# Performance work log

Measured on AMD Instinct MI355X. Metric: run time of the kernel, lower is better.

Reference implementation:

```python
import jax, jax.numpy as jnp
import numpy as np

D_IN = 768
D_OUT = 768
NUM_HEADS = 12
HEAD_DIM = D_OUT // NUM_HEADS
SEQ = 4096
BATCH = 1


def setup_inputs() -> dict:
    key = jax.random.key(0)
    ks = jax.random.split(key, 6)
    s = 1.0 / np.sqrt(D_IN)
    return {
        "x": jax.random.normal(ks[0], (BATCH, SEQ, D_IN), dtype=jnp.float32),
        "W_query": jax.random.normal(ks[1], (D_IN, D_OUT), dtype=jnp.float32) * s,
        "W_key": jax.random.normal(ks[2], (D_IN, D_OUT), dtype=jnp.float32) * s,
        "W_value": jax.random.normal(ks[3], (D_IN, D_OUT), dtype=jnp.float32) * s,
        "W_out": jax.random.normal(ks[4], (D_OUT, D_OUT), dtype=jnp.float32) * s,
        "b_out": jax.random.normal(ks[5], (D_OUT,), dtype=jnp.float32) * 0.01,
    }


def reference(x, W_query, W_key, W_value, W_out, b_out):
    B, S, _ = x.shape
    # QKV projections (qkv_bias=False)
    q = (x @ W_query).reshape(B, S, NUM_HEADS, HEAD_DIM)
    k = (x @ W_key).reshape(B, S, NUM_HEADS, HEAD_DIM)
    v = (x @ W_value).reshape(B, S, NUM_HEADS, HEAD_DIM)
    # attention scores [B, H, S, S] with causal mask
    scores = jnp.einsum("bqhd,bkhd->bhqk", q, k) / jnp.sqrt(
        jnp.asarray(HEAD_DIM, dtype=x.dtype)
    )
    causal = jnp.tril(jnp.ones((S, S), dtype=bool))
    scores = jnp.where(causal, scores, jnp.finfo(x.dtype).min)
    attn = jax.nn.softmax(scores, axis=-1)  # dropout p=0.0 -> identity
    ctx = jnp.einsum("bhqk,bkhd->bqhd", attn, v).reshape(B, S, D_OUT)
    return ctx @ W_out + b_out
```

## Files before the change

kernel.cpp:

```cpp
#include <hip/hip_runtime.h>
#include <stdint.h>

#define SEQ 4096
#define DM 768
#define NH 12
#define HD 64

typedef __attribute__((ext_vector_type(8))) short bf8;
typedef __attribute__((ext_vector_type(4))) float f4;
typedef __attribute__((ext_vector_type(16))) float f32x16;

static __device__ __forceinline__ f4 mfma_bf16(bf8 a, bf8 b, f4 c) {
  return __builtin_amdgcn_mfma_f32_16x16x32_bf16(a, b, c, 0, 0, 0);
}
static __device__ __forceinline__ f32x16 mfma32(bf8 a, bf8 b, f32x16 c) {
  return __builtin_amdgcn_mfma_f32_32x32x16_bf16(a, b, c, 0, 0, 0);
}

static __device__ __forceinline__ unsigned short f2bf(float f) {
  unsigned int u = __float_as_uint(f);
  u += 0x7FFFu + ((u >> 16) & 1u);
  return (unsigned short)(u >> 16);
}

static __device__ __forceinline__ unsigned int cvtpk(float lo, float hi) {
  unsigned int r;
  asm("v_cvt_pk_bf16_f32 %0, %1, %2" : "=v"(r) : "v"(lo), "v"(hi));
  return r;
}

static __device__ __forceinline__ void gload_lds16(const void* g, void* l) {
  __builtin_amdgcn_global_load_lds(
      (const __attribute__((address_space(1))) void*)g,
      (__attribute__((address_space(3))) void*)l, 16, 0, 0);
}

__global__ __launch_bounds__(256) void k_cvt(const float* __restrict__ x,
                                             unsigned short* __restrict__ xb) {
  int i = (blockIdx.x * 256 + threadIdx.x) * 4;
  float4 v = *reinterpret_cast<const float4*>(x + i);
  ushort4 o;
  o.x = f2bf(v.x); o.y = f2bf(v.y); o.z = f2bf(v.z); o.w = f2bf(v.w);
  *reinterpret_cast<ushort4*>(xb + i) = o;
}

__global__ __launch_bounds__(256) void k_tw(const float* __restrict__ w0,
                                            const float* __restrict__ w1,
                                            const float* __restrict__ w2,
                                            const float* __restrict__ w3,
                                            unsigned short* __restrict__ wt) {
  const float* W = blockIdx.z == 0 ? w0 : blockIdx.z == 1 ? w1
                 : blockIdx.z == 2 ? w2 : w3;
  unsigned short* WT = wt + (size_t)blockIdx.z * DM * DM;
  __shared__ float t[32][33];
  int c0 = blockIdx.x * 32, r0 = blockIdx.y * 32;
  int lx = threadIdx.x & 31, ly = threadIdx.x >> 5;
#pragma unroll
  for (int rr = 0; rr < 32; rr += 8)
    t[ly + rr][lx] = W[(size_t)(r0 + ly + rr) * DM + c0 + lx];
  __syncthreads();
#pragma unroll
  for (int rr = 0; rr < 32; rr += 8)
    WT[(size_t)(c0 + ly + rr) * DM + r0 + lx] = f2bf(t[lx][ly + rr]);
}

template <int MODE>
__global__ __launch_bounds__(256) void k_gemm2(const unsigned short* __restrict__ A,
                                               const unsigned short* __restrict__ Bt,
                                               unsigned short* __restrict__ Qh,
                                               unsigned short* __restrict__ Kh,
                                               unsigned short* __restrict__ Vtl,
                                               float* __restrict__ Cf,
                                               const float* __restrict__ bias,
                                               float qscale) {
  __shared__ unsigned short sA[128 * 32];
  __shared__ unsigned short sB[128 * 32];
  const int t = threadIdx.x, lane = t & 63, w = t >> 6;
  const int wr = w >> 1, wc = w & 1;
  const int c = lane & 15, g = lane >> 4;
  const int brow = blockIdx.x * 128, bcol = blockIdx.y * 128;
  f4 acc[4][4] = {};
  for (int k0 = 0; k0 < DM; k0 += 32) {
#pragma unroll
    for (int i = 0; i < 2; ++i) {
      int slot = w * 2 + i;
      int chunk = slot * 64 + lane;
      int row = chunk >> 2;
      int sl = (chunk & 3) ^ ((row >> 1) & 3);
      gload_lds16(A + (size_t)(brow + row) * DM + k0 + sl * 8, &sA[slot * 512]);
    }
#pragma unroll
    for (int i = 0; i < 2; ++i) {
      int slot = w * 2 + i;
      int chunk = slot * 64 + lane;
      int row = chunk >> 2;
      int sl = (chunk & 3) ^ ((row >> 1) & 3);
      gload_lds16(Bt + (size_t)(bcol + row) * DM + k0 + sl * 8, &sB[slot * 512]);
    }
    __syncthreads();
    bf8 af[4], bfr[4];
#pragma unroll
    for (int m = 0; m < 4; ++m) {
      int row = wr * 64 + m * 16 + c;
      int off = row * 64 + ((g * 16) ^ (((row >> 1) & 3) << 4));
      af[m] = *reinterpret_cast<const bf8*>(reinterpret_cast<const char*>(sA) + off);
    }
#pragma unroll
    for (int n = 0; n < 4; ++n) {
      int row = wc * 64 + n * 16 + c;
      int off = row * 64 + ((g * 16) ^ (((row >> 1) & 3) << 4));
      bfr[n] = *reinterpret_cast<const bf8*>(reinterpret_cast<const char*>(sB) + off);
    }
#pragma unroll
    for (int m = 0; m < 4; ++m)
#pragma unroll
      for (int n = 0; n < 4; ++n)
        acc[m][n] = mfma_bf16(af[m], bfr[n], acc[m][n]);
    __syncthreads();
  }
#pragma unroll
  for (int m = 0; m < 4; ++m) {
#pragma unroll
    for (int n = 0; n < 4; ++n) {
      int col = bcol + wc * 64 + n * 16 + c;
      int row0 = brow + wr * 64 + m * 16 + g * 4;
      if (MODE == 3) {
        int zone = col / 768;
        int ci = col - zone * 768;
        int h = ci >> 6, d = ci & 63;
        if (zone == 0) {
#pragma unroll
          for (int r = 0; r < 4; ++r)
            Qh[((size_t)h * SEQ + row0 + r) * 64 + d] = f2bf(acc[m][n][r] * qscale);
        } else if (zone == 1) {
#pragma unroll
          for (int r = 0; r < 4; ++r)
            Kh[((size_t)h * SEQ + row0 + r) * 64 + d] = f2bf(acc[m][n][r]);
        } else {
          ushort4 p;
          p.x = f2bf(acc[m][n][0]); p.y = f2bf(acc[m][n][1]);
          p.z = f2bf(acc[m][n][2]); p.w = f2bf(acc[m][n][3]);
          *reinterpret_cast<ushort4*>(
              Vtl + ((((size_t)h * 64 + (row0 >> 6)) * 64 + d) * 64 + (row0 & 63))) = p;
        }
      } else {
#pragma unroll
        for (int r = 0; r < 4; ++r)
          Cf[(size_t)(row0 + r) * DM + col] = acc[m][n][r] + bias[col];
      }
    }
  }
}

#define PSWAP(a, b) asm volatile("v_permlane32_swap_b32 %0, %1" : "+v"(a), "+v"(b))
#define SGB() __builtin_amdgcn_sched_barrier(0)

#define STAGE8K(srcbase, tile, dst) do {                                      \
    const unsigned short* s_ = (srcbase) + (size_t)(tile) * 4096 + kLaneOff;  \
    _Pragma("unroll")                                                         \
    for (int j_ = 0; j_ < 8; ++j_)                                            \
      gload_lds16(s_ + j_ * 512, (dst) + j_ * 1024);                          \
  } while (0)

#define PBUILD(sv, pfx, pfy) do {                                             \
    float p0_ = __builtin_amdgcn_exp2f(sv[0] - mn_);                          \
    float p1_ = __builtin_amdgcn_exp2f(sv[1] - mn_);                          \
    float p2_ = __builtin_amdgcn_exp2f(sv[2] - mn_);                          \
    float p3_ = __builtin_amdgcn_exp2f(sv[3] - mn_);                          \
    float p4_ = __builtin_amdgcn_exp2f(sv[4] - mn_);                          \
    float p5_ = __builtin_amdgcn_exp2f(sv[5] - mn_);                          \
    float p6_ = __builtin_amdgcn_exp2f(sv[6] - mn_);                          \
    float p7_ = __builtin_amdgcn_exp2f(sv[7] - mn_);                          \
    unsigned int wa0_ = cvtpk(p0_, p1_), wa1_ = cvtpk(p2_, p3_);              \
    unsigned int wb0_ = cvtpk(p4_, p5_), wb1_ = cvtpk(p6_, p7_);              \
    ls_ += ((p0_ + p1_) + (p2_ + p3_)) + ((p4_ + p5_) + (p6_ + p7_));         \
    float q0_ = __builtin_amdgcn_exp2f(sv[8] - mn_);                          \
    float q1_ = __builtin_amdgcn_exp2f(sv[9] - mn_);                          \
    float q2_ = __builtin_amdgcn_exp2f(sv[10] - mn_);                         \
    float q3_ = __builtin_amdgcn_exp2f(sv[11] - mn_);                         \
    float q4_ = __builtin_amdgcn_exp2f(sv[12] - mn_);                         \
    float q5_ = __builtin_amdgcn_exp2f(sv[13] - mn_);                         \
    float q6_ = __builtin_amdgcn_exp2f(sv[14] - mn_);                         \
    float q7_ = __builtin_amdgcn_exp2f(sv[15] - mn_);                         \
    unsigned int wc0_ = cvtpk(q0_, q1_), wc1_ = cvtpk(q2_, q3_);              \
    unsigned int wd0_ = cvtpk(q4_, q5_), wd1_ = cvtpk(q6_, q7_);              \
    ls_ += ((q0_ + q1_) + (q2_ + q3_)) + ((q4_ + q5_) + (q6_ + q7_));         \
    PSWAP(wa0_, wb0_);                                                        \
    PSWAP(wa1_, wb1_);                                                        \
    PSWAP(wc0_, wd0_);                                                        \
    PSWAP(wc1_, wd1_);                                                        \
    uint4 u0_ = {wa0_, wa1_, wb0_, wb1_};                                     \
    uint4 u1_ = {wc0_, wc1_, wd0_, wd1_};                                     \
    pfx = *reinterpret_cast<bf8*>(&u0_);                                      \
    pfy = *reinterpret_cast<bf8*>(&u1_);                                      \
  } while (0)

#define FMAX8(v, i0) fmaxf(fmaxf(fmaxf(v[i0], v[i0+1]), fmaxf(v[i0+2], v[i0+3])), \
                           fmaxf(fmaxf(v[i0+4], v[i0+5]), fmaxf(v[i0+6], v[i0+7])))

#define XHALF_MAX(x) do {                                                     \
    float cp_ = (x);                                                          \
    asm volatile("" : "+v"(cp_));                                             \
    PSWAP((x), cp_);                                                          \
    (x) = fmaxf((x), cp_);                                                    \
  } while (0)
#define XHALF_ADD(x) do {                                                     \
    float cp_ = (x);                                                          \
    asm volatile("" : "+v"(cp_));                                             \
    PSWAP((x), cp_);                                                          \
    (x) = (x) + cp_;                                                          \
  } while (0)

#define STEP64(t, stage_) do {                                                \
    asm volatile("s_waitcnt vmcnt(0)" ::: "memory");                          \
    SGB();                                                                    \
    const int x0_ = ((hi) ^ xq) << 4;                                         \
    const int x1_ = ((2 + hi) ^ xq) << 4;                                     \
    const int x2_ = ((4 + hi) ^ xq) << 4;                                     \
    const int x3_ = ((6 + hi) ^ xq) << 4;                                     \
    const char* kr0_ = kbuf + ql * 128;                                       \
    const char* kr1_ = kbuf + (32 + ql) * 128;                                \
    bf8 ka0_ = *(const bf8*)(kr0_ + x0_);                                     \
    bf8 kb0_ = *(const bf8*)(kr1_ + x0_);                                     \
    bf8 ka1_ = *(const bf8*)(kr0_ + x1_);                                     \
    bf8 kb1_ = *(const bf8*)(kr1_ + x1_);                                     \
    bf8 ka2_ = *(const bf8*)(kr0_ + x2_);                                     \
    bf8 kb2_ = *(const bf8*)(kr1_ + x2_);                                     \
    bf8 ka3_ = *(const bf8*)(kr0_ + x3_);                                     \
    bf8 kb3_ = *(const bf8*)(kr1_ + x3_);                                     \
    SGB();                                                                    \
    asm volatile("s_waitcnt lgkmcnt(0)" ::: "memory");                        \
    SGB();                                                                    \
    if (stage_) STAGE8K(Khp, (t) + 4, kbuf);                                  \
    f32x16 s0_ = {}, s1_ = {};                                                \
    __builtin_amdgcn_s_setprio(1);                                            \
    s0_ = mfma32(ka0_, qf[0], s0_);  s1_ = mfma32(kb0_, qf[0], s1_);          \
    s0_ = mfma32(ka1_, qf[1], s0_);  s1_ = mfma32(kb1_, qf[1], s1_);          \
    s0_ = mfma32(ka2_, qf[2], s0_);  s1_ = mfma32(kb2_, qf[2], s1_);          \
    s0_ = mfma32(ka3_, qf[3], s0_);  s1_ = mfma32(kb3_, qf[3], s1_);          \
    __builtin_amdgcn_s_setprio(0);                                            \
    if ((t) == dt) {                                                          \
      _Pragma("unroll")                                                       \
      for (int r_ = 0; r_ < 16; ++r_) {                                       \
        int kr_ = (t) * 64 + (r_ & 3) + 8 * (r_ >> 2) + 4 * hi;               \
        s0_[r_] = (kr_ > qg) ? -1e30f : s0_[r_];                              \
        s1_[r_] = (kr_ + 32 > qg) ? -1e30f : s1_[r_];                         \
      }                                                                       \
    }                                                                         \
    float tm_ = fmaxf(fmaxf(FMAX8(s0_, 0), FMAX8(s0_, 8)),                    \
                      fmaxf(FMAX8(s1_, 0), FMAX8(s1_, 8)));                   \
    XHALF_MAX(tm_);                                                           \
    float mn_, al_;                                                           \
    if (__all(tm_ <= m + 8.f)) {                                              \
      mn_ = m;                                                                \
      al_ = 1.0f;                                                             \
    } else {                                                                  \
      mn_ = fmaxf(m, tm_);                                                    \
      al_ = __builtin_amdgcn_exp2f(m - mn_);                                  \
      m = mn_;                                                                \
      _Pragma("unroll")                                                       \
      for (int r_ = 0; r_ < 16; ++r_) { o0[r_] *= al_; o1[r_] *= al_; }       \
    }                                                                         \
    float ls_ = 0.f;                                                          \
    bf8 pfA0_, pfA1_, pfB0_, pfB1_;                                           \
    PBUILD(s0_, pfA0_, pfA1_);                                                \
    PBUILD(s1_, pfB0_, pfB1_);                                                \
    XHALF_ADD(ls_);                                                           \
    l = l * al_ + ls_;                                                        \
    const char* vr0_ = vbuf + ql * 128;                                       \
    const char* vr1_ = vbuf + (32 + ql) * 128;                                \
    bf8 va0_ = *(const bf8*)(vr0_ + x0_);                                     \
    bf8 va1_ = *(const bf8*)(vr0_ + x1_);                                     \
    bf8 va2_ = *(const bf8*)(vr0_ + x2_);                                     \
    bf8 va3_ = *(const bf8*)(vr0_ + x3_);                                     \
    bf8 vb0_ = *(const bf8*)(vr1_ + x0_);                                     \
    bf8 vb1_ = *(const bf8*)(vr1_ + x1_);                                     \
    bf8 vb2_ = *(const bf8*)(vr1_ + x2_);                                     \
    bf8 vb3_ = *(const bf8*)(vr1_ + x3_);                                     \
    SGB();                                                                    \
    asm volatile("s_waitcnt lgkmcnt(0)" ::: "memory");                        \
    SGB();                                                                    \
    if (stage_) STAGE8K(Vtp, (t) + 4, vbuf);                                  \
    __builtin_amdgcn_s_setprio(1);                                            \
    o0 = mfma32(va0_, pfA0_, o0);                                             \
    o0 = mfma32(va1_, pfA1_, o0);                                             \
    o0 = mfma32(va2_, pfB0_, o0);                                             \
    o0 = mfma32(va3_, pfB1_, o0);                                             \
    o1 = mfma32(vb0_, pfA0_, o1);                                             \
    o1 = mfma32(vb1_, pfA1_, o1);                                             \
    o1 = mfma32(vb2_, pfB0_, o1);                                             \
    o1 = mfma32(vb3_, pfB1_, o1);                                             \
    __builtin_amdgcn_s_setprio(0);                                            \
  } while (0)

__global__ __launch_bounds__(256, 2) void k_attn(const unsigned short* __restrict__ Qh,
                                                 const unsigned short* __restrict__ Kh,
                                                 const unsigned short* __restrict__ Vt,
                                                 unsigned short* __restrict__ ctx) {
  const int tid = threadIdx.x;
  const int lane = tid & 63;
  const int w = tid >> 6;
  const int ql = lane & 31, hi = lane >> 5;
  const int xq = ql & 7;

  const int L = (int)blockIdx.x;
  const int W = (L & 7) * 96 + (L >> 3);
  const int h = W >> 6;
  const int b = W & 63;

  __shared__ __align__(16) char smem[66560];
  char* kbuf = smem + w * 8192;
  char* vbuf = smem + 32768 + w * 8192;
  float* sO = (float*)smem;
  float* sM = (float*)(smem + 65536);
  float* sL = (float*)(smem + 66048);

  const unsigned short* Khp = Kh + (size_t)h * SEQ * 64;
  const unsigned short* Qhp = Qh + (size_t)h * SEQ * 64;
  const unsigned short* Vtp = Vt + (size_t)h * SEQ * 64;
  const int kLaneOff = (lane >> 3) * 64 + ((lane & 7) ^ (lane >> 3)) * 8;

  for (int ph = 0; ph < 2; ++ph) {
    const int qt = ph ? (127 - b) : b;
    const int qg = qt * 32 + ql;
    const int dt = qt >> 1;
    bf8 qf[4];
    {
      const unsigned short* qp = Qhp + (size_t)qg * 64 + hi * 8;
      qf[0] = *reinterpret_cast<const bf8*>(qp);
      qf[1] = *reinterpret_cast<const bf8*>(qp + 16);
      qf[2] = *reinterpret_cast<const bf8*>(qp + 32);
      qf[3] = *reinterpret_cast<const bf8*>(qp + 48);
    }
    f32x16 o0 = {}, o1 = {};
    float m = -1e30f, l = 0.f;

    const int nt = (dt >= w) ? ((dt - w) >> 2) + 1 : 0;
    if (nt > 0) {
      STAGE8K(Khp, w, kbuf);
      STAGE8K(Vtp, w, vbuf);
      for (int i = 0; i < nt; ++i) {
        const int t = w + 4 * i;
        STEP64(t, (i + 1 < nt));
      }
    }
    __syncthreads();

#pragma unroll
    for (int r = 0; r < 16; ++r) {
      int dr = (r & 3) + 8 * (r >> 2) + 4 * hi;
      sO[w * 2048 + dr * 32 + ql] = o0[r];
      sO[w * 2048 + (32 + dr) * 32 + ql] = o1[r];
    }
    if (hi == 0) { sM[w * 32 + ql] = m; sL[w * 32 + ql] = l; }
    __syncthreads();
    {
      const int q = tid & 31;
      const int dblk = tid >> 5;
      float m0 = sM[q], m1 = sM[32 + q], m2 = sM[64 + q], m3 = sM[96 + q];
      float mn = fmaxf(fmaxf(m0, m1), fmaxf(m2, m3));
      float a0 = __builtin_amdgcn_exp2f(m0 - mn);
      float a1 = __builtin_amdgcn_exp2f(m1 - mn);
      float a2 = __builtin_amdgcn_exp2f(m2 - mn);
      float a3 = __builtin_amdgcn_exp2f(m3 - mn);
      float inv = 1.f / (a0 * sL[q] + a1 * sL[32 + q] + a2 * sL[64 + q] + a3 * sL[96 + q]);
      a0 *= inv; a1 *= inv; a2 *= inv; a3 *= inv;
      unsigned short* cp = ctx + (size_t)(qt * 32 + q) * DM + h * HD + dblk * 8;
#pragma unroll
      for (int j = 0; j < 8; j += 2) {
        int d = dblk * 8 + j;
        float v0 = sO[d * 32 + q] * a0 + sO[2048 + d * 32 + q] * a1 +
                   sO[4096 + d * 32 + q] * a2 + sO[6144 + d * 32 + q] * a3;
        float v1 = sO[(d + 1) * 32 + q] * a0 + sO[2048 + (d + 1) * 32 + q] * a1 +
                   sO[4096 + (d + 1) * 32 + q] * a2 + sO[6144 + (d + 1) * 32 + q] * a3;
        *reinterpret_cast<unsigned int*>(cp + j) = cvtpk(v0, v1);
      }
    }
    __syncthreads();
  }
}

extern "C" void kernel_launch(void* const* d_in, const int* in_sizes, int n_in,
                              void* d_out, int out_size, void* d_ws, size_t ws_size,
                              hipStream_t stream) {
  const float* x  = (const float*)d_in[0];
  const float* Wq = (const float*)d_in[1];
  const float* Wk = (const float*)d_in[2];
  const float* Wv = (const float*)d_in[3];
  const float* Wo = (const float*)d_in[4];
  const float* bo = (const float*)d_in[5];

  unsigned short* xb = (unsigned short*)d_ws;
  unsigned short* wt = xb + (size_t)SEQ * DM;
  unsigned short* Qh = wt + (size_t)4 * DM * DM;
  unsigned short* Kh = Qh + (size_t)SEQ * DM;
  unsigned short* Vt = Kh + (size_t)SEQ * DM;
  unsigned short* cx = Vt + (size_t)SEQ * DM;

  const float qscale = 1.4426950408889634f / 8.0f;

  k_cvt<<<(SEQ * DM) / 1024, 256, 0, stream>>>(x, xb);
  k_tw<<<dim3(24, 24, 4), 256, 0, stream>>>(Wq, Wk, Wv, Wo, wt);
  k_gemm2<3><<<dim3(SEQ / 128, 2304 / 128), 256, 0, stream>>>(
      xb, wt, Qh, Kh, Vt, nullptr, nullptr, qscale);
  k_attn<<<dim3(768), 256, 0, stream>>>(Qh, Kh, Vt, cx);
  k_gemm2<2><<<dim3(SEQ / 128, DM / 128), 256, 0, stream>>>(
      cx, wt + (size_t)3 * DM * DM, nullptr, nullptr, nullptr,
      (float*)d_out, bo, 1.0f);
}
```

Baseline: 120.1 us.

## Shrink attention key/value tile to 32 rows and raise occupancy to four blocks

The attention inner loop now processes 32 keys per step instead of 64, halving per-wave K/V staging buffers and total LDS. This lets launch bounds request four blocks per CU instead of two. The V projection epilogue writes a new 32-row transposed tile layout with a matching XOR-swizzled staging path. The aim is more resident waves to hide latency and less masked work on the causal diagonal, at the cost of twice as many loop iterations, each with its own waits, max/sum reductions and rescaling.

Measured after the change: 120.8 us. About the same (+0.5%).

```diff
diff --git a/kernel.cpp b/kernel.cpp
--- a/kernel.cpp
+++ b/kernel.cpp
@@ -141,7 +141,7 @@
           p.x = f2bf(acc[m][n][0]); p.y = f2bf(acc[m][n][1]);
           p.z = f2bf(acc[m][n][2]); p.w = f2bf(acc[m][n][3]);
           *reinterpret_cast<ushort4*>(
-              Vtl + ((((size_t)h * 64 + (row0 >> 6)) * 64 + d) * 64 + (row0 & 63))) = p;
+              Vtl + ((((size_t)h * 128 + (row0 >> 5)) * 64 + d) * 32 + (row0 & 31))) = p;
         }
       } else {
 #pragma unroll
@@ -155,11 +155,21 @@
 #define PSWAP(a, b) asm volatile("v_permlane32_swap_b32 %0, %1" : "+v"(a), "+v"(b))
 #define SGB() __builtin_amdgcn_sched_barrier(0)
 
-#define STAGE8K(srcbase, tile, dst) do {                                      \
-    const unsigned short* s_ = (srcbase) + (size_t)(tile) * 4096 + kLaneOff;  \
+#define STAGE4K(srcbase, tile, dst) do {                                      \
+    const unsigned short* s_ = (srcbase) + (size_t)(tile) * 2048 + kLaneOffK; \
     _Pragma("unroll")                                                         \
-    for (int j_ = 0; j_ < 8; ++j_)                                            \
+    for (int j_ = 0; j_ < 4; ++j_)                                            \
       gload_lds16(s_ + j_ * 512, (dst) + j_ * 1024);                          \
+  } while (0)
+
+#define STAGE4KV(srcbase, tile, dst) do {                                     \
+    const unsigned short* s_ = (srcbase) + (size_t)(tile) * 2048;             \
+    _Pragma("unroll")                                                         \
+    for (int j_ = 0; j_ < 4; ++j_) {                                          \
+      int c_ = (lane & 3) ^ ((lane >> 2) & 3) ^ ((lane >> 4) & 3) ^ j_;       \
+      gload_lds16(s_ + j_ * 512 + (lane >> 2) * 32 + c_ * 8,                  \
+                  (dst) + j_ * 1024);                                         \
+    }                                                                         \
   } while (0)
 
 #define PBUILD(sv, pfx, pfy) do {                                             \
@@ -211,44 +221,33 @@
     (x) = (x) + cp_;                                                          \
   } while (0)
 
-#define STEP64(t, stage_) do {                                                \
+#define STEP32(t, stage_) do {                                                \
     asm volatile("s_waitcnt vmcnt(0)" ::: "memory");                          \
     SGB();                                                                    \
-    const int x0_ = ((hi) ^ xq) << 4;                                         \
-    const int x1_ = ((2 + hi) ^ xq) << 4;                                     \
-    const int x2_ = ((4 + hi) ^ xq) << 4;                                     \
-    const int x3_ = ((6 + hi) ^ xq) << 4;                                     \
     const char* kr0_ = kbuf + ql * 128;                                       \
-    const char* kr1_ = kbuf + (32 + ql) * 128;                                \
-    bf8 ka0_ = *(const bf8*)(kr0_ + x0_);                                     \
-    bf8 kb0_ = *(const bf8*)(kr1_ + x0_);                                     \
-    bf8 ka1_ = *(const bf8*)(kr0_ + x1_);                                     \
-    bf8 kb1_ = *(const bf8*)(kr1_ + x1_);                                     \
-    bf8 ka2_ = *(const bf8*)(kr0_ + x2_);                                     \
-    bf8 kb2_ = *(const bf8*)(kr1_ + x2_);                                     \
-    bf8 ka3_ = *(const bf8*)(kr0_ + x3_);                                     \
-    bf8 kb3_ = *(const bf8*)(kr1_ + x3_);                                     \
+    bf8 ka0_ = *(const bf8*)(kr0_ + (((hi) ^ xq) << 4));                      \
+    bf8 ka1_ = *(const bf8*)(kr0_ + (((2 + hi) ^ xq) << 4));                  \
+    bf8 ka2_ = *(const bf8*)(kr0_ + (((4 + hi) ^ xq) << 4));                  \
+    bf8 ka3_ = *(const bf8*)(kr0_ + (((6 + hi) ^ xq) << 4));                  \
     SGB();                                                                    \
     asm volatile("s_waitcnt lgkmcnt(0)" ::: "memory");                        \
     SGB();                                                                    \
-    if (stage_) STAGE8K(Khp, (t) + 4, kbuf);                                  \
-    f32x16 s0_ = {}, s1_ = {};                                                \
+    if (stage_) STAGE4K(Khp, (t) + 4, kbuf);                                  \
+    f32x16 s0_ = {};                                                          \
     __builtin_amdgcn_s_setprio(1);                                            \
-    s0_ = mfma32(ka0_, qf[0], s0_);  s1_ = mfma32(kb0_, qf[0], s1_);          \
-    s0_ = mfma32(ka1_, qf[1], s0_);  s1_ = mfma32(kb1_, qf[1], s1_);          \
-    s0_ = mfma32(ka2_, qf[2], s0_);  s1_ = mfma32(kb2_, qf[2], s1_);          \
-    s0_ = mfma32(ka3_, qf[3], s0_);  s1_ = mfma32(kb3_, qf[3], s1_);          \
+    s0_ = mfma32(ka0_, qf[0], s0_);                                           \
+    s0_ = mfma32(ka1_, qf[1], s0_);                                           \
+    s0_ = mfma32(ka2_, qf[2], s0_);                                           \
+    s0_ = mfma32(ka3_, qf[3], s0_);                                           \
     __builtin_amdgcn_s_setprio(0);                                            \
     if ((t) == dt) {                                                          \
       _Pragma("unroll")                                                       \
       for (int r_ = 0; r_ < 16; ++r_) {                                       \
-        int kr_ = (t) * 64 + (r_ & 3) + 8 * (r_ >> 2) + 4 * hi;               \
+        int kr_ = (t) * 32 + (r_ & 3) + 8 * (r_ >> 2) + 4 * hi;               \
         s0_[r_] = (kr_ > qg) ? -1e30f : s0_[r_];                              \
-        s1_[r_] = (kr_ + 32 > qg) ? -1e30f : s1_[r_];                         \
       }                                                                       \
     }                                                                         \
-    float tm_ = fmaxf(fmaxf(FMAX8(s0_, 0), FMAX8(s0_, 8)),                    \
-                      fmaxf(FMAX8(s1_, 0), FMAX8(s1_, 8)));                   \
+    float tm_ = fmaxf(FMAX8(s0_, 0), FMAX8(s0_, 8));                          \
     XHALF_MAX(tm_);                                                           \
     float mn_, al_;                                                           \
     if (__all(tm_ <= m + 8.f)) {                                              \
@@ -262,38 +261,27 @@
       for (int r_ = 0; r_ < 16; ++r_) { o0[r_] *= al_; o1[r_] *= al_; }       \
     }                                                                         \
     float ls_ = 0.f;                                                          \
-    bf8 pfA0_, pfA1_, pfB0_, pfB1_;                                           \
+    bf8 pfA0_, pfA1_;                                                         \
     PBUILD(s0_, pfA0_, pfA1_);                                                \
-    PBUILD(s1_, pfB0_, pfB1_);                                                \
     XHALF_ADD(ls_);                                                           \
     l = l * al_ + ls_;                                                        \
-    const char* vr0_ = vbuf + ql * 128;                                       \
-    const char* vr1_ = vbuf + (32 + ql) * 128;                                \
-    bf8 va0_ = *(const bf8*)(vr0_ + x0_);                                     \
-    bf8 va1_ = *(const bf8*)(vr0_ + x1_);                                     \
-    bf8 va2_ = *(const bf8*)(vr0_ + x2_);                                     \
-    bf8 va3_ = *(const bf8*)(vr0_ + x3_);                                     \
-    bf8 vb0_ = *(const bf8*)(vr1_ + x0_);                                     \
-    bf8 vb1_ = *(const bf8*)(vr1_ + x1_);                                     \
-    bf8 vb2_ = *(const bf8*)(vr1_ + x2_);                                     \
-    bf8 vb3_ = *(const bf8*)(vr1_ + x3_);                                     \
+    bf8 va0_ = *(const bf8*)(vbuf + ql * 64 + (((hi) ^ prA) << 4));           \
+    bf8 va1_ = *(const bf8*)(vbuf + ql * 64 + (((2 + hi) ^ prA) << 4));       \
+    bf8 vb0_ = *(const bf8*)(vbuf + (32 + ql) * 64 + (((hi) ^ prB) << 4));    \
+    bf8 vb1_ = *(const bf8*)(vbuf + (32 + ql) * 64 + (((2 + hi) ^ prB) << 4));\
     SGB();                                                                    \
     asm volatile("s_waitcnt lgkmcnt(0)" ::: "memory");                        \
     SGB();                                                                    \
-    if (stage_) STAGE8K(Vtp, (t) + 4, vbuf);                                  \
+    if (stage_) STAGE4KV(Vtp, (t) + 4, vbuf);                                 \
     __builtin_amdgcn_s_setprio(1);                                            \
     o0 = mfma32(va0_, pfA0_, o0);                                             \
     o0 = mfma32(va1_, pfA1_, o0);                                             \
-    o0 = mfma32(va2_, pfB0_, o0);                                             \
-    o0 = mfma32(va3_, pfB1_, o0);                                             \
     o1 = mfma32(vb0_, pfA0_, o1);                                             \
     o1 = mfma32(vb1_, pfA1_, o1);                                             \
-    o1 = mfma32(vb2_, pfB0_, o1);                                             \
-    o1 = mfma32(vb3_, pfB1_, o1);                                             \
     __builtin_amdgcn_s_setprio(0);                                            \
   } while (0)
 
-__global__ __launch_bounds__(256, 2) void k_attn(const unsigned short* __restrict__ Qh,
+__global__ __launch_bounds__(256, 4) void k_attn(const unsigned short* __restrict__ Qh,
                                                  const unsigned short* __restrict__ Kh,
                                                  const unsigned short* __restrict__ Vt,
                                                  unsigned short* __restrict__ ctx) {
@@ -302,28 +290,30 @@
   const int w = tid >> 6;
   const int ql = lane & 31, hi = lane >> 5;
   const int xq = ql & 7;
+  const int prA = (ql & 3) ^ ((ql >> 2) & 3) ^ ((ql >> 4) & 3);
+  const int prB = prA ^ 2;
 
   const int L = (int)blockIdx.x;
   const int W = (L & 7) * 96 + (L >> 3);
   const int h = W >> 6;
   const int b = W & 63;
 
-  __shared__ __align__(16) char smem[66560];
-  char* kbuf = smem + w * 8192;
-  char* vbuf = smem + 32768 + w * 8192;
+  __shared__ __align__(16) char smem[33792];
+  char* kbuf = smem + w * 4096;
+  char* vbuf = smem + 16384 + w * 4096;
   float* sO = (float*)smem;
-  float* sM = (float*)(smem + 65536);
-  float* sL = (float*)(smem + 66048);
+  float* sM = (float*)(smem + 32768);
+  float* sL = (float*)(smem + 33280);
 
   const unsigned short* Khp = Kh + (size_t)h * SEQ * 64;
   const unsigned short* Qhp = Qh + (size_t)h * SEQ * 64;
   const unsigned short* Vtp = Vt + (size_t)h * SEQ * 64;
-  const int kLaneOff = (lane >> 3) * 64 + ((lane & 7) ^ (lane >> 3)) * 8;
+  const int kLaneOffK = (lane >> 3) * 64 + ((lane & 7) ^ (lane >> 3)) * 8;
 
   for (int ph = 0; ph < 2; ++ph) {
     const int qt = ph ? (127 - b) : b;
     const int qg = qt * 32 + ql;
-    const int dt = qt >> 1;
+    const int dt = qt;
     bf8 qf[4];
     {
       const unsigned short* qp = Qhp + (size_t)qg * 64 + hi * 8;
@@ -337,11 +327,11 @@
 
     const int nt = (dt >= w) ? ((dt - w) >> 2) + 1 : 0;
     if (nt > 0) {
-      STAGE8K(Khp, w, kbuf);
-      STAGE8K(Vtp, w, vbuf);
+      STAGE4K(Khp, w, kbuf);
+      STAGE4KV(Vtp, w, vbuf);
       for (int i = 0; i < nt; ++i) {
         const int t = w + 4 * i;
-        STEP64(t, (i + 1 < nt));
+        STEP32(t, (i + 1 < nt));
       }
     }
     __syncthreads();
```
